# Kernel tuning notes

Measured on AMD Instinct MI355X. Metric: run time of the kernel, lower is better.

The kernel has to match this reference:

```python
import jax, jax.numpy as jnp
import numpy as np

N_EMBD = 1024
N_HEAD = 16
LATENT = 64
HEAD_DIM = N_EMBD // N_HEAD
B, T = 2, 2048
SCALE = 1.0 / np.sqrt(LATENT)


def setup_inputs() -> dict:
    key = jax.random.key(0)
    ks = jax.random.split(key, 10)
    s = lambda fan_in: 1.0 / np.sqrt(fan_in)
    return {
        "x": jax.random.normal(ks[0], (B, T, N_EMBD), dtype=jnp.float32),
        "Wq": jax.random.normal(ks[1], (N_EMBD, N_EMBD), dtype=jnp.float32) * s(N_EMBD),
        "bq": jnp.zeros((N_EMBD,), dtype=jnp.float32),
        "Wk": jax.random.normal(ks[2], (N_EMBD, N_HEAD * LATENT), dtype=jnp.float32) * s(N_EMBD),
        "bk": jnp.zeros((N_HEAD * LATENT,), dtype=jnp.float32),
        "Wv": jax.random.normal(ks[3], (N_EMBD, N_HEAD * LATENT), dtype=jnp.float32) * s(N_EMBD),
        "bv": jnp.zeros((N_HEAD * LATENT,), dtype=jnp.float32),
        "Wo": jax.random.normal(ks[4], (N_HEAD * LATENT, N_EMBD), dtype=jnp.float32) * s(N_HEAD * LATENT),
        "bo": jnp.zeros((N_EMBD,), dtype=jnp.float32),
        "Wc": jax.random.normal(ks[5], (HEAD_DIM, LATENT), dtype=jnp.float32) * s(HEAD_DIM),
    }


def reference(x, Wq, bq, Wk, bk, Wv, bv, Wo, bo, Wc):
    Bv, Tv, C = x.shape
    # projections
    q = (x @ Wq + bq).reshape(Bv, Tv, N_HEAD, HEAD_DIM)        # [B,T,H,Dh]
    k = (x @ Wk + bk).reshape(Bv, Tv, N_HEAD, LATENT)          # [B,T,H,L]
    v = (x @ Wv + bv).reshape(Bv, Tv, N_HEAD, LATENT)          # [B,T,H,L]
    # compress q into latent dim: [B,T,H,L]
    qc = jnp.einsum("bthd,dl->bthl", q, Wc)
    # attention scores [B,H,T,T]
    att = jnp.einsum("bthl,bshl->bhts", qc, k) * SCALE
    causal = jnp.tril(jnp.ones((Tv, Tv), dtype=bool))
    att = jnp.where(causal[None, None], att, -jnp.inf)
    att = jax.nn.softmax(att, axis=-1)
    y = jnp.einsum("bhts,bshl->bthl", att, v).reshape(Bv, Tv, N_HEAD * LATENT)
    return y @ Wo + bo
```

## Files before the change

kernel.cpp:

```cpp
#include <hip/hip_runtime.h>
#include <stdint.h>

#define TT 2048
#define BB 2
#define MROWS (BB*TT)
#define SCALEF 0.125f
#define LSCALE 0.18033688011112043f

typedef unsigned short u16;
typedef __bf16 bf16x8 __attribute__((ext_vector_type(8)));
typedef float f32x4 __attribute__((ext_vector_type(4)));
typedef short s16x8 __attribute__((ext_vector_type(8)));
typedef unsigned short u16x4 __attribute__((ext_vector_type(4)));

#define GLOBAL_AS const __attribute__((address_space(1))) void*
#define LDS_AS __attribute__((address_space(3))) void*

__device__ __forceinline__ u16 f2b(float f){
  uint32_t u = __builtin_bit_cast(uint32_t, f);
  u = (u + 0x7FFFu + ((u >> 16) & 1u)) >> 16;
  return (u16)u;
}

__global__ void cvt_bf16(const float* __restrict__ in, u16* __restrict__ out, int n4){
  int i = blockIdx.x * 256 + threadIdx.x;
  if (i < n4){
    float4 v = ((const float4*)in)[i];
    u16x4 o; o.x = f2b(v.x); o.y = f2b(v.y); o.z = f2b(v.z); o.w = f2b(v.w);
    ((u16x4*)out)[i] = o;
  }
}

__global__ __launch_bounds__(256) void build_wqc(const float* __restrict__ Wq,
                                                 const float* __restrict__ Wc,
                                                 float* __restrict__ Wqc){
  __shared__ float wc[4096];
  const int t = threadIdx.x;
  #pragma unroll
  for (int i = 0; i < 16; ++i) wc[i * 256 + t] = Wc[i * 256 + t];
  __syncthreads();
  const int idx = blockIdx.x * 256 + t;
  const int d = idx >> 6;
  const int h = (idx >> 2) & 15;
  const int lq = idx & 3;
  float wqr[64];
  const float4* wq4 = (const float4*)(Wq + (size_t)d * 1024 + h * 64);
  #pragma unroll
  for (int i = 0; i < 16; ++i){
    float4 v = wq4[i];
    wqr[i * 4 + 0] = v.x; wqr[i * 4 + 1] = v.y; wqr[i * 4 + 2] = v.z; wqr[i * 4 + 3] = v.w;
  }
  float* outp = Wqc + (size_t)d * 1024 + h * 64 + lq * 16;
  #pragma unroll
  for (int j = 0; j < 16; ++j){
    int lc = lq * 16 + j;
    float acc = 0.f;
    #pragma unroll
    for (int dd = 0; dd < 64; ++dd) acc += wqr[dd] * wc[dd * 64 + lc];
    outp[j] = acc;
  }
}

__global__ void build_bqc(const float* __restrict__ bq, const float* __restrict__ Wc,
                          float* __restrict__ bqc){
  int n = blockIdx.x * 256 + threadIdx.x;
  int h = n >> 6, lc = n & 63;
  float acc = 0.f;
  for (int dd = 0; dd < 64; ++dd) acc += bq[h * 64 + dd] * Wc[dd * 64 + lc];
  bqc[n] = acc;
}

__global__ void transpose_w4(const float* __restrict__ s0, const float* __restrict__ s1,
                             const float* __restrict__ s2, const float* __restrict__ s3,
                             u16* __restrict__ o0, u16* __restrict__ o1,
                             u16* __restrict__ o2, u16* __restrict__ o3){
  const int z = blockIdx.z;
  const float* in = (z == 0) ? s0 : (z == 1) ? s1 : (z == 2) ? s2 : s3;
  u16* out = (z == 0) ? o0 : (z == 1) ? o1 : (z == 2) ? o2 : o3;
  __shared__ float t[32][33];
  int tx = threadIdx.x & 31, ty = threadIdx.x >> 5;
  int c0 = blockIdx.x * 32, r0 = blockIdx.y * 32;
  #pragma unroll
  for (int i = 0; i < 32; i += 8)
    t[ty + i][tx] = in[(size_t)(r0 + ty + i) * 1024 + c0 + tx];
  __syncthreads();
  #pragma unroll
  for (int i = 0; i < 32; i += 8)
    out[(size_t)(c0 + ty + i) * 1024 + r0 + tx] = f2b(t[tx][ty + i]);
}

__global__ void transpose_v(const u16* __restrict__ vb, u16* __restrict__ vt){
  __shared__ u16 t[32][34];
  int tx = threadIdx.x & 31, ty = threadIdx.x >> 5;
  int s0 = blockIdx.x * 32, d0 = blockIdx.y * 32, bh = blockIdx.z;
  int b = bh >> 4, h = bh & 15;
  #pragma unroll
  for (int i = 0; i < 32; i += 8)
    t[ty + i][tx] = vb[(size_t)(b * TT + s0 + ty + i) * 1024 + h * 64 + d0 + tx];
  __syncthreads();
  #pragma unroll
  for (int i = 0; i < 32; i += 8)
    vt[((size_t)bh * 64 + d0 + ty + i) * TT + s0 + tx] = t[tx][ty + i];
}

__device__ __forceinline__ void gemm_tile(const u16* __restrict__ A, const u16* __restrict__ BT,
                                          int m0, int n0, int K, f32x4 (&acc)[4][4],
                                          u16* As, u16* Bs, int tid){
  const int wv = tid >> 6, l = tid & 63;
  const int aoff = ((wv >> 1) * 64 + (l & 15)) * 32 + ((l >> 4) << 3);
  const int boff = ((wv & 1) * 64 + (l & 15)) * 32 + ((l >> 4) << 3);
  const int ob0 = wv * 1024 + l * 16;
  for (int kt = 0; kt < K; kt += 32){
    __syncthreads();
    #pragma unroll
    for (int j = 0; j < 2; ++j){
      int ob = ob0 + j * 4096;
      int row = ob >> 6, col = (ob & 63) >> 1;
      __builtin_amdgcn_global_load_lds((GLOBAL_AS)(A + (size_t)(m0 + row) * 1024 + kt + col),
                                       (LDS_AS)(As + wv * 512 + j * 2048), 16, 0, 0);
      __builtin_amdgcn_global_load_lds((GLOBAL_AS)(BT + (size_t)(n0 + row) * 1024 + kt + col),
                                       (LDS_AS)(Bs + wv * 512 + j * 2048), 16, 0, 0);
    }
    __syncthreads();
    bf16x8 av[4], bw[4];
    #pragma unroll
    for (int m = 0; m < 4; ++m) av[m] = *(const bf16x8*)(As + aoff + m * 512);
    #pragma unroll
    for (int n = 0; n < 4; ++n) bw[n] = *(const bf16x8*)(Bs + boff + n * 512);
    #pragma unroll
    for (int m = 0; m < 4; ++m)
      #pragma unroll
      for (int n = 0; n < 4; ++n)
        acc[m][n] = __builtin_amdgcn_mfma_f32_16x16x32_bf16(av[m], bw[n], acc[m][n], 0, 0, 0);
  }
}

__global__ __launch_bounds__(256) void gemm_qkv(
    const u16* __restrict__ xb,
    const u16* __restrict__ W0T, const u16* __restrict__ W1T, const u16* __restrict__ W2T,
    const float* __restrict__ b0, const float* __restrict__ b1, const float* __restrict__ b2,
    u16* __restrict__ o0, u16* __restrict__ o1, u16* __restrict__ o2){
  __shared__ u16 As[4096], Bs[4096];
  const int z = blockIdx.z;
  const u16* BT = (z == 0) ? W0T : (z == 1) ? W1T : W2T;
  const float* bias = (z == 0) ? b0 : (z == 1) ? b1 : b2;
  u16* Out = (z == 0) ? o0 : (z == 1) ? o1 : o2;
  const int n0 = blockIdx.x * 128, m0 = blockIdx.y * 128;
  const int tid = threadIdx.x, wv = tid >> 6, l = tid & 63;
  f32x4 acc[4][4] = {};
  gemm_tile(xb, BT, m0, n0, 1024, acc, As, Bs, tid);
  const int wr = wv >> 1, wc = wv & 1;
  #pragma unroll
  for (int n = 0; n < 4; ++n){
    int col = n0 + wc * 64 + n * 16 + (l & 15);
    float bb = bias[col];
    #pragma unroll
    for (int m = 0; m < 4; ++m){
      int r0 = m0 + wr * 64 + m * 16 + ((l >> 4) << 2);
      #pragma unroll
      for (int r = 0; r < 4; ++r)
        Out[(size_t)(r0 + r) * 1024 + col] = f2b(acc[m][n][r] + bb);
    }
  }
}

__global__ __launch_bounds__(256) void gemm_fp32out(
    const u16* __restrict__ A, const u16* __restrict__ BT,
    const float* __restrict__ bias, float* __restrict__ Out){
  __shared__ u16 As[4096], Bs[4096];
  const int n0 = blockIdx.x * 128, m0 = blockIdx.y * 128;
  const int tid = threadIdx.x, wv = tid >> 6, l = tid & 63;
  f32x4 acc[4][4] = {};
  gemm_tile(A, BT, m0, n0, 1024, acc, As, Bs, tid);
  const int wr = wv >> 1, wc = wv & 1;
  #pragma unroll
  for (int n = 0; n < 4; ++n){
    int col = n0 + wc * 64 + n * 16 + (l & 15);
    float bb = bias[col];
    #pragma unroll
    for (int m = 0; m < 4; ++m){
      int r0 = m0 + wr * 64 + m * 16 + ((l >> 4) << 2);
      #pragma unroll
      for (int r = 0; r < 4; ++r)
        Out[(size_t)(r0 + r) * 1024 + col] = acc[m][n][r] + bb;
    }
  }
}

__global__ __launch_bounds__(512) void attn(
    const u16* __restrict__ qcg, const u16* __restrict__ kg,
    const u16* __restrict__ vtg, u16* __restrict__ yg){
  __shared__ u16 Ks[2][4096], Vs[2][4096];
  __shared__ u16 Ps[8 * 16 * 72];
  const int idx = blockIdx.x;
  const int qt = 15 - (idx >> 5), bh = idx & 31;
  const int b = bh >> 4, h = bh & 15;
  const int q0 = qt * 128;
  const int tid = threadIdx.x, wv = tid >> 6, l = tid & 63;
  const int c4 = l >> 4;
  const size_t base = (size_t)b * TT * 1024 + h * 64;
  const u16* Q = qcg + base;
  const u16* K = kg + base;
  const u16* Vt = vtg + (size_t)bh * 64 * TT;

  const int sr = tid >> 3;
  const int sc = (tid & 7) ^ (sr & 7);
  const u16* gK = K + (size_t)sr * 1024 + sc * 8;
  const u16* gV = Vt + (size_t)sr * TT + sc * 8;

  __builtin_amdgcn_global_load_lds((GLOBAL_AS)gK, (LDS_AS)(&Ks[0][0] + wv * 512), 16, 0, 0);
  __builtin_amdgcn_global_load_lds((GLOBAL_AS)gV, (LDS_AS)(&Vs[0][0] + wv * 512), 16, 0, 0);

  bf16x8 qf[2];
  {
    int qr = q0 + wv * 16 + (l & 15);
    #pragma unroll
    for (int ks = 0; ks < 2; ++ks)
      qf[ks] = *(const bf16x8*)(Q + (size_t)qr * 1024 + ks * 32 + (c4 << 3));
  }
  f32x4 yacc[4] = {};
  float mrow = -1e30f, srow = 0.f;

  const int nt = 2 * qt + 2;
  for (int st = 0; st < nt; ++st){
    const int cur = st & 1;
    const u16* Kc = &Ks[cur][0];
    const u16* Vc = &Vs[cur][0];
    if (st + 1 < nt){
      const int s1 = (st + 1) * 64;
      __builtin_amdgcn_global_load_lds((GLOBAL_AS)(gK + (size_t)s1 * 1024),
                                       (LDS_AS)(&Ks[cur ^ 1][0] + wv * 512), 16, 0, 0);
      __builtin_amdgcn_global_load_lds((GLOBAL_AS)(gV + s1),
                                       (LDS_AS)(&Vs[cur ^ 1][0] + wv * 512), 16, 0, 0);
      asm volatile("s_waitcnt vmcnt(2)" ::: "memory");
    } else {
      asm volatile("s_waitcnt vmcnt(0)" ::: "memory");
    }
    __builtin_amdgcn_sched_barrier(0);
    __builtin_amdgcn_s_barrier();
    __builtin_amdgcn_sched_barrier(0);
    const int s0 = st * 64;
    f32x4 sf[4] = {};
    __builtin_amdgcn_s_setprio(1);
    #pragma unroll
    for (int ks = 0; ks < 2; ++ks)
      #pragma unroll
      for (int nf = 0; nf < 4; ++nf){
        int r = nf * 16 + (l & 15), c = ks * 4 + c4;
        bf16x8 kf = *(const bf16x8*)(Kc + (r * 8 + (c ^ (r & 7))) * 8);
        sf[nf] = __builtin_amdgcn_mfma_f32_16x16x32_bf16(kf, qf[ks], sf[nf], 0, 0, 0);
      }
    __builtin_amdgcn_s_setprio(0);
    const int qa = q0 + wv * 16 + (l & 15);
    float p[4][4];
    const bool domask = (s0 + 63 > q0 + wv * 16);
    #pragma unroll
    for (int nf = 0; nf < 4; ++nf)
      #pragma unroll
      for (int r = 0; r < 4; ++r){
        float v_ = sf[nf][r] * LSCALE;
        if (domask && (s0 + nf * 16 + c4 * 4 + r > qa)) v_ = -1e30f;
        p[nf][r] = v_;
      }
    float tmax = p[0][0];
    #pragma unroll
    for (int nf = 0; nf < 4; ++nf)
      #pragma unroll
      for (int r = 0; r < 4; ++r) tmax = fmaxf(tmax, p[nf][r]);
    tmax = fmaxf(tmax, __shfl_xor(tmax, 16));
    tmax = fmaxf(tmax, __shfl_xor(tmax, 32));
    if (__any(tmax > mrow + 8.0f)){
      float mnew = fmaxf(mrow, tmax);
      float resc = exp2f(mrow - mnew);
      srow *= resc;
      mrow = mnew;
      float rq[4];
      #pragma unroll
      for (int r = 0; r < 4; ++r) rq[r] = __shfl(resc, (l & 48) | (c4 * 4 + r));
      #pragma unroll
      for (int df = 0; df < 4; ++df)
        #pragma unroll
        for (int r = 0; r < 4; ++r) yacc[df][r] *= rq[r];
    }
    float tsum = 0.f;
    #pragma unroll
    for (int nf = 0; nf < 4; ++nf)
      #pragma unroll
      for (int r = 0; r < 4; ++r){ float e = exp2f(p[nf][r] - mrow); p[nf][r] = e; tsum += e; }
    tsum += __shfl_xor(tsum, 16);
    tsum += __shfl_xor(tsum, 32);
    srow += tsum;
    {
      uint32_t* dst = (uint32_t*)(Ps + wv * 1152 + (l & 15) * 72);
      #pragma unroll
      for (int nf = 0; nf < 4; ++nf){
        uint32_t w0, w1;
        asm volatile("v_cvt_pk_bf16_f32 %0, %1, %2" : "=v"(w0) : "v"(p[nf][0]), "v"(p[nf][1]));
        asm volatile("v_cvt_pk_bf16_f32 %0, %1, %2" : "=v"(w1) : "v"(p[nf][2]), "v"(p[nf][3]));
        *(uint64_t*)(dst + nf * 8 + c4 * 2) = (uint64_t)w0 | ((uint64_t)w1 << 32);
      }
    }
    asm volatile("s_waitcnt lgkmcnt(0)" ::: "memory");
    __builtin_amdgcn_sched_barrier(0);
    __builtin_amdgcn_s_setprio(1);
    #pragma unroll
    for (int ks2 = 0; ks2 < 2; ++ks2){
      bf16x8 pf = *(const bf16x8*)(Ps + wv * 1152 + (l & 15) * 72 + ks2 * 32 + c4 * 8);
      #pragma unroll
      for (int df = 0; df < 4; ++df){
        int rd = df * 16 + (l & 15), cd = ks2 * 4 + c4;
        bf16x8 vf = *(const bf16x8*)(Vc + (rd * 8 + (cd ^ (rd & 7))) * 8);
        yacc[df] = __builtin_amdgcn_mfma_f32_16x16x32_bf16(pf, vf, yacc[df], 0, 0, 0);
      }
    }
    __builtin_amdgcn_s_setprio(0);
    __builtin_amdgcn_s_barrier();
  }
  float sq[4];
  #pragma unroll
  for (int r = 0; r < 4; ++r) sq[r] = __shfl(srow, (l & 48) | (c4 * 4 + r));
  #pragma unroll
  for (int df = 0; df < 4; ++df){
    int d = df * 16 + (l & 15);
    int qq = q0 + wv * 16 + c4 * 4;
    #pragma unroll
    for (int r = 0; r < 4; ++r){
      float val = yacc[df][r] / sq[r];
      yg[(size_t)(b * TT + qq + r) * 1024 + h * 64 + d] = f2b(val);
    }
  }
}

extern "C" void kernel_launch(void* const* d_in, const int* in_sizes, int n_in,
                              void* d_out, int out_size, void* d_ws, size_t ws_size,
                              hipStream_t stream){
  (void)in_sizes; (void)n_in; (void)out_size; (void)ws_size;
  const float* x  = (const float*)d_in[0];
  const float* Wq = (const float*)d_in[1];
  const float* bq = (const float*)d_in[2];
  const float* Wk = (const float*)d_in[3];
  const float* bk = (const float*)d_in[4];
  const float* Wv = (const float*)d_in[5];
  const float* bv = (const float*)d_in[6];
  const float* Wo = (const float*)d_in[7];
  const float* bo = (const float*)d_in[8];
  const float* Wc = (const float*)d_in[9];
  float* out = (float*)d_out;

  char* wsb = (char*)d_ws;
  u16* xb    = (u16*)(wsb);
  u16* yb    = (u16*)(wsb);
  u16* qcb   = (u16*)(wsb + (8u  << 20));
  u16* kb    = (u16*)(wsb + (16u << 20));
  u16* vb    = (u16*)(wsb + (24u << 20));
  u16* vtb   = (u16*)(wsb + (32u << 20));
  u16* WqcT  = (u16*)(wsb + (40u << 20));
  u16* WkT   = (u16*)(wsb + (42u << 20));
  u16* WvT   = (u16*)(wsb + (44u << 20));
  u16* WoT   = (u16*)(wsb + (46u << 20));
  float* bqc  = (float*)(wsb + (48u << 20));
  float* Wqcf = (float*)(wsb + (48u << 20) + 8192);

  cvt_bf16<<<4096, 256, 0, stream>>>(x, xb, MROWS * 1024 / 4);
  build_wqc<<<256, 256, 0, stream>>>(Wq, Wc, Wqcf);
  build_bqc<<<4, 256, 0, stream>>>(bq, Wc, bqc);
  transpose_w4<<<dim3(32, 32, 4), 256, 0, stream>>>(Wqcf, Wk, Wv, Wo, WqcT, WkT, WvT, WoT);
  gemm_qkv<<<dim3(8, 32, 3), 256, 0, stream>>>(xb, WqcT, WkT, WvT, bqc, bk, bv, qcb, kb, vb);
  transpose_v<<<dim3(64, 2, 32), 256, 0, stream>>>(vb, vtb);
  attn<<<dim3(512), 512, 0, stream>>>(qcb, kb, vtb, yb);
  gemm_fp32out<<<dim3(8, 32), 256, 0, stream>>>(yb, WoT, bo, out);
}
```

Measured before the change: 140.9 us.

## Use 64-row query tiles in attention with 4 waves and swizzled P buffer

The attention kernel now processes 64 query rows per block with 256 threads (1024 blocks) instead of 128 rows with 512 threads. Each wave loads two K/V chunks per stage, so the block count doubles and causal waste per block shrinks. The softmax log2 scale is folded into the Q projection epilogue, and masking is applied only on the final diagonal tile. The P staging buffer drops its padding in favour of an XOR swizzle to avoid bank conflicts. The trade-off is more blocks that each reload K/V, which doubles K/V global traffic.

```diff
diff --git a/kernel.cpp b/kernel.cpp
--- a/kernel.cpp
+++ b/kernel.cpp
@@ -4,7 +4,6 @@
 #define TT 2048
 #define BB 2
 #define MROWS (BB*TT)
-#define SCALEF 0.125f
 #define LSCALE 0.18033688011112043f
 
 typedef unsigned short u16;
@@ -145,6 +144,7 @@
   const u16* BT = (z == 0) ? W0T : (z == 1) ? W1T : W2T;
   const float* bias = (z == 0) ? b0 : (z == 1) ? b1 : b2;
   u16* Out = (z == 0) ? o0 : (z == 1) ? o1 : o2;
+  const float osc = (z == 0) ? LSCALE : 1.0f;
   const int n0 = blockIdx.x * 128, m0 = blockIdx.y * 128;
   const int tid = threadIdx.x, wv = tid >> 6, l = tid & 63;
   f32x4 acc[4][4] = {};
@@ -159,7 +159,7 @@
       int r0 = m0 + wr * 64 + m * 16 + ((l >> 4) << 2);
       #pragma unroll
       for (int r = 0; r < 4; ++r)
-        Out[(size_t)(r0 + r) * 1024 + col] = f2b(acc[m][n][r] + bb);
+        Out[(size_t)(r0 + r) * 1024 + col] = f2b((acc[m][n][r] + bb) * osc);
     }
   }
 }
@@ -187,17 +187,17 @@
   }
 }
 
-__global__ __launch_bounds__(512) void attn(
+__global__ __launch_bounds__(256) void attn(
     const u16* __restrict__ qcg, const u16* __restrict__ kg,
     const u16* __restrict__ vtg, u16* __restrict__ yg){
   __shared__ u16 Ks[2][4096], Vs[2][4096];
-  __shared__ u16 Ps[8 * 16 * 72];
+  __shared__ u16 Ps[4 * 16 * 64];
   const int idx = blockIdx.x;
-  const int qt = 15 - (idx >> 5), bh = idx & 31;
+  const int qt = 31 - (idx >> 5), bh = idx & 31;
   const int b = bh >> 4, h = bh & 15;
-  const int q0 = qt * 128;
+  const int q0 = qt * 64;
   const int tid = threadIdx.x, wv = tid >> 6, l = tid & 63;
-  const int c4 = l >> 4;
+  const int c4 = l >> 4, q16 = l & 15;
   const size_t base = (size_t)b * TT * 1024 + h * 64;
   const u16* Q = qcg + base;
   const u16* K = kg + base;
@@ -209,11 +209,13 @@
   const u16* gV = Vt + (size_t)sr * TT + sc * 8;
 
   __builtin_amdgcn_global_load_lds((GLOBAL_AS)gK, (LDS_AS)(&Ks[0][0] + wv * 512), 16, 0, 0);
+  __builtin_amdgcn_global_load_lds((GLOBAL_AS)(gK + 32 * 1024), (LDS_AS)(&Ks[0][0] + 2048 + wv * 512), 16, 0, 0);
   __builtin_amdgcn_global_load_lds((GLOBAL_AS)gV, (LDS_AS)(&Vs[0][0] + wv * 512), 16, 0, 0);
+  __builtin_amdgcn_global_load_lds((GLOBAL_AS)(gV + 32 * TT), (LDS_AS)(&Vs[0][0] + 2048 + wv * 512), 16, 0, 0);
 
   bf16x8 qf[2];
   {
-    int qr = q0 + wv * 16 + (l & 15);
+    int qr = q0 + wv * 16 + q16;
     #pragma unroll
     for (int ks = 0; ks < 2; ++ks)
       qf[ks] = *(const bf16x8*)(Q + (size_t)qr * 1024 + ks * 32 + (c4 << 3));
@@ -221,18 +223,23 @@
   f32x4 yacc[4] = {};
   float mrow = -1e30f, srow = 0.f;
 
-  const int nt = 2 * qt + 2;
+  uint32_t* const PsW = (uint32_t*)Ps + wv * 512 + q16 * 32;
+  const int pm = (q16 & 7) << 2;
+
+  const int nt = qt + 1;
   for (int st = 0; st < nt; ++st){
     const int cur = st & 1;
     const u16* Kc = &Ks[cur][0];
     const u16* Vc = &Vs[cur][0];
     if (st + 1 < nt){
       const int s1 = (st + 1) * 64;
-      __builtin_amdgcn_global_load_lds((GLOBAL_AS)(gK + (size_t)s1 * 1024),
-                                       (LDS_AS)(&Ks[cur ^ 1][0] + wv * 512), 16, 0, 0);
-      __builtin_amdgcn_global_load_lds((GLOBAL_AS)(gV + s1),
-                                       (LDS_AS)(&Vs[cur ^ 1][0] + wv * 512), 16, 0, 0);
-      asm volatile("s_waitcnt vmcnt(2)" ::: "memory");
+      u16* kd = &Ks[cur ^ 1][0] + wv * 512;
+      u16* vd = &Vs[cur ^ 1][0] + wv * 512;
+      __builtin_amdgcn_global_load_lds((GLOBAL_AS)(gK + (size_t)s1 * 1024), (LDS_AS)kd, 16, 0, 0);
+      __builtin_amdgcn_global_load_lds((GLOBAL_AS)(gK + (size_t)(s1 + 32) * 1024), (LDS_AS)(kd + 2048), 16, 0, 0);
+      __builtin_amdgcn_global_load_lds((GLOBAL_AS)(gV + s1), (LDS_AS)vd, 16, 0, 0);
+      __builtin_amdgcn_global_load_lds((GLOBAL_AS)(gV + s1 + 32 * TT), (LDS_AS)(vd + 2048), 16, 0, 0);
+      asm volatile("s_waitcnt vmcnt(4)" ::: "memory");
     } else {
       asm volatile("s_waitcnt vmcnt(0)" ::: "memory");
     }
@@ -246,19 +253,19 @@
     for (int ks = 0; ks < 2; ++ks)
       #pragma unroll
       for (int nf = 0; nf < 4; ++nf){
-        int r = nf * 16 + (l & 15), c = ks * 4 + c4;
+        int r = nf * 16 + q16, c = ks * 4 + c4;
         bf16x8 kf = *(const bf16x8*)(Kc + (r * 8 + (c ^ (r & 7))) * 8);
         sf[nf] = __builtin_amdgcn_mfma_f32_16x16x32_bf16(kf, qf[ks], sf[nf], 0, 0, 0);
       }
     __builtin_amdgcn_s_setprio(0);
-    const int qa = q0 + wv * 16 + (l & 15);
+    const int qa = q0 + wv * 16 + q16;
     float p[4][4];
-    const bool domask = (s0 + 63 > q0 + wv * 16);
+    const bool domask = (st == nt - 1);
     #pragma unroll
     for (int nf = 0; nf < 4; ++nf)
       #pragma unroll
       for (int r = 0; r < 4; ++r){
-        float v_ = sf[nf][r] * LSCALE;
+        float v_ = sf[nf][r];
         if (domask && (s0 + nf * 16 + c4 * 4 + r > qa)) v_ = -1e30f;
         p[nf][r] = v_;
       }
@@ -290,25 +297,22 @@
     tsum += __shfl_xor(tsum, 16);
     tsum += __shfl_xor(tsum, 32);
     srow += tsum;
-    {
-      uint32_t* dst = (uint32_t*)(Ps + wv * 1152 + (l & 15) * 72);
-      #pragma unroll
-      for (int nf = 0; nf < 4; ++nf){
-        uint32_t w0, w1;
-        asm volatile("v_cvt_pk_bf16_f32 %0, %1, %2" : "=v"(w0) : "v"(p[nf][0]), "v"(p[nf][1]));
-        asm volatile("v_cvt_pk_bf16_f32 %0, %1, %2" : "=v"(w1) : "v"(p[nf][2]), "v"(p[nf][3]));
-        *(uint64_t*)(dst + nf * 8 + c4 * 2) = (uint64_t)w0 | ((uint64_t)w1 << 32);
-      }
+    #pragma unroll
+    for (int nf = 0; nf < 4; ++nf){
+      uint32_t w0, w1;
+      asm volatile("v_cvt_pk_bf16_f32 %0, %1, %2" : "=v"(w0) : "v"(p[nf][0]), "v"(p[nf][1]));
+      asm volatile("v_cvt_pk_bf16_f32 %0, %1, %2" : "=v"(w1) : "v"(p[nf][2]), "v"(p[nf][3]));
+      *(uint64_t*)(PsW + ((nf * 8 + c4 * 2) ^ pm)) = (uint64_t)w0 | ((uint64_t)w1 << 32);
     }
     asm volatile("s_waitcnt lgkmcnt(0)" ::: "memory");
     __builtin_amdgcn_sched_barrier(0);
     __builtin_amdgcn_s_setprio(1);
     #pragma unroll
     for (int ks2 = 0; ks2 < 2; ++ks2){
-      bf16x8 pf = *(const bf16x8*)(Ps + wv * 1152 + (l & 15) * 72 + ks2 * 32 + c4 * 8);
+      bf16x8 pf = *(const bf16x8*)(PsW + ((ks2 * 16 + c4 * 4) ^ pm));
       #pragma unroll
       for (int df = 0; df < 4; ++df){
-        int rd = df * 16 + (l & 15), cd = ks2 * 4 + c4;
+        int rd = df * 16 + q16, cd = ks2 * 4 + c4;
         bf16x8 vf = *(const bf16x8*)(Vc + (rd * 8 + (cd ^ (rd & 7))) * 8);
         yacc[df] = __builtin_amdgcn_mfma_f32_16x16x32_bf16(pf, vf, yacc[df], 0, 0, 0);
       }
@@ -321,7 +325,7 @@
   for (int r = 0; r < 4; ++r) sq[r] = __shfl(srow, (l & 48) | (c4 * 4 + r));
   #pragma unroll
   for (int df = 0; df < 4; ++df){
-    int d = df * 16 + (l & 15);
+    int d = df * 16 + q16;
     int qq = q0 + wv * 16 + c4 * 4;
     #pragma unroll
     for (int r = 0; r < 4; ++r){
@@ -367,6 +371,6 @@
   transpose_w4<<<dim3(32, 32, 4), 256, 0, stream>>>(Wqcf, Wk, Wv, Wo, WqcT, WkT, WvT, WoT);
   gemm_qkv<<<dim3(8, 32, 3), 256, 0, stream>>>(xb, WqcT, WkT, WvT, bqc, bk, bv, qcb, kb, vb);
   transpose_v<<<dim3(64, 2, 32), 256, 0, stream>>>(vb, vtb);
-  attn<<<dim3(512), 512, 0, stream>>>(qcb, kb, vtb, yb);
+  attn<<<dim3(1024), 256, 0, stream>>>(qcb, kb, vtb, yb);
   gemm_fp32out<<<dim3(8, 32), 256, 0, stream>>>(yb, WoT, bo, out);
 }
```

Result: faster. 131.4 us (-6.8%).
